# Kernel optimization log

Hardware: AMD Instinct MI355X
Metric: run time of the kernel (lower is better)

## Reference

```python
import jax, jax.numpy as jnp
import numpy as np
import math

B = 2; T = 512; ND = 256; NDAYS = 24; STRIDE = 4; KLEN = 14
DM = ND * KLEN          # 3584, d_model after unfolding
NLAYERS = 2; DSTATE = 16; DCONV = 4; EXPAND = 2
DI = EXPAND * DM        # 7168 d_inner
DTR = math.ceil(DM / 16)  # 224 dt_rank
NCLS = 41
LOUT = (T - KLEN) // STRIDE + 1  # 125


def setup_inputs():
    key = jax.random.key(0)
    ks = jax.random.split(key, 12)
    f32 = jnp.float32
    neuralInput = jax.random.normal(ks[0], (B, T, ND), f32)
    dayIdx = jax.random.randint(ks[1], (B,), 0, NDAYS)
    # day-specific linear init: identity weight, zero bias (as in BaseDecoder)
    day_w = jnp.tile(jnp.eye(ND, dtype=f32)[None], (NDAYS, 1, 1))
    day_b = jnp.zeros((NDAYS, 1, ND), f32)
    norm_w = jnp.ones((NLAYERS, DM), f32)
    norm_b = jnp.zeros((NLAYERS, DM), f32)
    in_proj_w = 0.02 * jax.random.normal(ks[2], (NLAYERS, 2 * DI, DM), f32)
    conv_w = 0.2 * jax.random.normal(ks[3], (NLAYERS, DI, DCONV), f32)  # depthwise
    conv_b = jnp.zeros((NLAYERS, DI), f32)
    x_proj_w = 0.02 * jax.random.normal(ks[4], (NLAYERS, DTR + 2 * DSTATE, DI), f32)
    s = DTR ** -0.5
    dt_proj_w = jax.random.uniform(ks[5], (NLAYERS, DI, DTR), f32, -s, s)
    # dt bias init: inverse-softplus of dt ~ LogUniform[1e-3, 1e-1]
    dt = jnp.exp(jax.random.uniform(ks[6], (NLAYERS, DI), f32) * (math.log(0.1) - math.log(0.001)) + math.log(0.001))
    dt = jnp.clip(dt, 1e-4, None)
    dt_proj_b = dt + jnp.log(-jnp.expm1(-dt))
    A_log = jnp.broadcast_to(jnp.log(jnp.arange(1, DSTATE + 1, dtype=f32)), (NLAYERS, DI, DSTATE)).copy()
    D_param = jnp.ones((NLAYERS, DI), f32)
    out_proj_w = 0.02 * jax.random.normal(ks[7], (NLAYERS, DM, DI), f32)
    normf_w = jnp.ones((DM,), f32)
    normf_b = jnp.zeros((DM,), f32)
    fc_w = 0.02 * jax.random.normal(ks[8], (NCLS, DM), f32)
    fc_b = jnp.zeros((NCLS,), f32)
    return dict(neuralInput=neuralInput, day_w=day_w, day_b=day_b, norm_w=norm_w, norm_b=norm_b,
                in_proj_w=in_proj_w, conv_w=conv_w, conv_b=conv_b, x_proj_w=x_proj_w,
                dt_proj_w=dt_proj_w, dt_proj_b=dt_proj_b, A_log=A_log, D_param=D_param,
                out_proj_w=out_proj_w, normf_w=normf_w, normf_b=normf_b, fc_w=fc_w, fc_b=fc_b,
                dayIdx=dayIdx)


def _layernorm(x, w, b):
    mu = x.mean(-1, keepdims=True)
    v = jnp.var(x, -1, keepdims=True)
    return (x - mu) * jax.lax.rsqrt(v + 1e-5) * w + b


def _mamba(h, ipw, cw, cb, xpw, dtw, dtb, Alog, Dp, opw):
    # h: (B, L, DM) -> (B, L, DM); unidirectional Mamba, use_fast_path=False math
    Bb, L, _ = h.shape
    xz = h @ ipw.T                              # (B, L, 2*DI)
    x, z = xz[..., :DI], xz[..., DI:]
    # depthwise causal conv1d, kernel DCONV, left pad DCONV-1, truncated to L
    xp = jnp.pad(x, ((0, 0), (DCONV - 1, 0), (0, 0)))
    xc = cb + sum(xp[:, j:j + L, :] * cw[:, j] for j in range(DCONV))
    x = jax.nn.silu(xc)
    x_dbl = x @ xpw.T                           # (B, L, DTR + 2*N)
    dt = x_dbl[..., :DTR]
    Bc = x_dbl[..., DTR:DTR + DSTATE]
    Cc = x_dbl[..., DTR + DSTATE:]
    delta = jax.nn.softplus(dt @ dtw.T + dtb)   # (B, L, DI), delta_softplus=True
    A = -jnp.exp(Alog)                          # (DI, N)
    dA = jnp.exp(delta[..., None] * A)          # (B, L, DI, N)
    dBu = (delta * x)[..., None] * Bc[:, :, None, :]  # (B, L, DI, N)

    def step(hst, inp):
        a, bu, c = inp
        hst = a * hst + bu                      # (B, DI, N)
        return hst, jnp.einsum('bdn,bn->bd', hst, c)

    h0 = jnp.zeros((Bb, DI, DSTATE), h.dtype)
    _, ys = jax.lax.scan(step, h0, (dA.transpose(1, 0, 2, 3), dBu.transpose(1, 0, 2, 3), Cc.transpose(1, 0, 2)))
    y = ys.transpose(1, 0, 2) + x * Dp          # skip term D*u
    y = y * jax.nn.silu(z)                      # gated output
    return y @ opw.T


def reference(neuralInput, day_w, day_b, norm_w, norm_b, in_proj_w, conv_w, conv_b, x_proj_w,
              dt_proj_w, dt_proj_b, A_log, D_param, out_proj_w, normf_w, normf_b, fc_w, fc_b, dayIdx):
    # --- BaseDecoder.forward_preprocessing (gaussianSmoothWidth = 0) ---
    t = jnp.einsum('btd,bdk->btk', neuralInput, day_w[dayIdx]) + day_b[dayIdx]
    t = t / (1.0 + jnp.abs(t))                  # Softsign
    idx = jnp.arange(LOUT)[:, None] * STRIDE + jnp.arange(KLEN)[None, :]
    win = t[:, idx, :]                          # (B, LOUT, KLEN, ND)
    # torch Unfold feature ordering: channel-major then kernel position -> d*KLEN + j
    h = win.transpose(0, 1, 3, 2).reshape(t.shape[0], LOUT, DM)
    # --- stacked Mamba blocks (pre-norm residual) ---
    residual = None
    for i in range(NLAYERS):
        residual = h if residual is None else h + residual
        hn = _layernorm(residual, norm_w[i], norm_b[i])
        h = _mamba(hn, in_proj_w[i], conv_w[i], conv_b[i], x_proj_w[i], dt_proj_w[i],
                   dt_proj_b[i], A_log[i], D_param[i], out_proj_w[i])
    residual = h + residual
    hn = _layernorm(residual, normf_w, normf_b)
    return hn @ fc_w.T + fc_b                   # (B, LOUT, NCLS)
```

## Files before the change

### kernel.cpp

```cpp
#include <hip/hip_runtime.h>
#include <hip/hip_bf16.h>
#include <math.h>

#define BATCH   2
#define TSEQ    512
#define NDIM    256
#define STRIDE_ 4
#define KLEN    14
#define DM      3584
#define DI      7168
#define DTR     224
#define DSTATE  16
#define NCLS    41
#define LOUT    125
#define LPAD    128
#define MROWS   256

typedef __attribute__((ext_vector_type(8))) short bf8_t;
typedef __attribute__((ext_vector_type(4))) float f4_t;

__device__ inline unsigned bfpair(float a, float b) {
    unsigned ua = __builtin_bit_cast(unsigned, a);
    unsigned ub = __builtin_bit_cast(unsigned, b);
    ua = (ua + 0x7fffu + ((ua >> 16) & 1u)) >> 16;
    ub = (ub + 0x7fffu + ((ub >> 16) & 1u)) >> 16;
    return ua | (ub << 16);
}
__device__ inline uint4 pack8(float4 a, float4 b) {
    return make_uint4(bfpair(a.x, a.y), bfpair(a.z, a.w),
                      bfpair(b.x, b.y), bfpair(b.z, b.w));
}

__global__ void day_proj(const float* __restrict__ nI, const float* __restrict__ dw,
                         const float* __restrict__ db, const int* __restrict__ dayIdx,
                         float* __restrict__ t_full) {
    int bi = blockIdx.x;
    int b = bi >> 9;
    int di = dayIdx[b];
    int tid = threadIdx.x;
    __shared__ float a_sh[256];
    a_sh[tid] = nI[(size_t)bi * 256 + tid];
    __syncthreads();
    const float* w = dw + (size_t)di * 65536;
    float acc = db[(size_t)di * 256 + tid];
    #pragma unroll 8
    for (int d = 0; d < 256; ++d) acc = fmaf(a_sh[d], w[d * 256 + tid], acc);
    t_full[(size_t)bi * 256 + tid] = acc / (1.f + fabsf(acc));
}

__global__ void window_k(const float* __restrict__ t_full, float* __restrict__ res) {
    int bl = blockIdx.x;
    int b = bl >> 7, l = bl & 127;
    size_t m = (size_t)b * LPAD + l;
    if (l >= LOUT) {
        for (int c = threadIdx.x; c < DM; c += 256) res[m * DM + c] = 0.f;
        return;
    }
    for (int c = threadIdx.x; c < DM; c += 256) {
        int d = c / KLEN, j = c - d * KLEN;
        res[m * DM + c] = t_full[((size_t)b * TSEQ + l * STRIDE_ + j) * 256 + d];
    }
}

template <bool ADD>
__global__ void ln_pack(float* __restrict__ res, const float* __restrict__ part,
                        const float* __restrict__ w, const float* __restrict__ b,
                        short* __restrict__ hnp) {
    __shared__ __align__(16) float hs[DM];
    __shared__ float sm[8];
    int m = blockIdx.x, tid = threadIdx.x;
    float* row = res + (size_t)m * DM;
    float s = 0.f, ss = 0.f;
    for (int c = tid; c < DM; c += 256) {
        float v = row[c];
        if (ADD) {
            v += part[((size_t)0 * MROWS + m) * DM + c]
               + part[((size_t)1 * MROWS + m) * DM + c]
               + part[((size_t)2 * MROWS + m) * DM + c]
               + part[((size_t)3 * MROWS + m) * DM + c];
            row[c] = v;
        }
        hs[c] = v; s += v; ss += v * v;
    }
    #pragma unroll
    for (int o = 32; o; o >>= 1) { s += __shfl_xor(s, o); ss += __shfl_xor(ss, o); }
    int wid = tid >> 6;
    if ((tid & 63) == 0) { sm[wid] = s; sm[4 + wid] = ss; }
    __syncthreads();
    s = sm[0] + sm[1] + sm[2] + sm[3];
    ss = sm[4] + sm[5] + sm[6] + sm[7];
    float mu = s * (1.f / DM);
    float var = ss * (1.f / DM) - mu * mu;
    float rs = rsqrtf(var + 1e-5f);
    for (int G = tid; G < DM / 8; G += 256) {
        float4 f0 = *(const float4*)(hs + G * 8);
        float4 f1 = *(const float4*)(hs + G * 8 + 4);
        float4 w0 = *(const float4*)(w + G * 8);
        float4 w1 = *(const float4*)(w + G * 8 + 4);
        float4 b0 = *(const float4*)(b + G * 8);
        float4 b1 = *(const float4*)(b + G * 8 + 4);
        f0.x = (f0.x - mu) * rs * w0.x + b0.x; f0.y = (f0.y - mu) * rs * w0.y + b0.y;
        f0.z = (f0.z - mu) * rs * w0.z + b0.z; f0.w = (f0.w - mu) * rs * w0.w + b0.w;
        f1.x = (f1.x - mu) * rs * w1.x + b1.x; f1.y = (f1.y - mu) * rs * w1.y + b1.y;
        f1.z = (f1.z - mu) * rs * w1.z + b1.z; f1.w = (f1.w - mu) * rs * w1.w + b1.w;
        *(uint4*)&hnp[((size_t)G * 256 + m) * 8] = pack8(f0, f1);
    }
}

template <int EPI, int NT>
__global__ __launch_bounds__(256)
void gemm_mfma(const short* __restrict__ Ap, const float* __restrict__ W, int ldw,
               float* __restrict__ C, int ldc, int kSteps, size_t cStrideZ,
               const float* __restrict__ bias) {
    constexpr int NC = NT / 16;
    __shared__ __align__(16) short a_sh[3][4][2056];
    __shared__ __align__(16) short w_sh[3][4][NT * 8 + 8];
    const int tid = threadIdx.x;
    const int wz = tid >> 6, lane = tid & 63;
    const int g = lane >> 4, i16 = lane & 15;
    const int n0 = blockIdx.x * NT;
    const int sBeg = blockIdx.z * kSteps, sEnd = sBeg + kSteps;
    const int wr = tid >> 3;
    const int wq = tid & 7;
    C += (size_t)blockIdx.z * cStrideZ;

    f4_t acc[4][NC];
    #pragma unroll
    for (int r = 0; r < 4; ++r)
        #pragma unroll
        for (int c = 0; c < NC; ++c) acc[r][c] = (f4_t){0.f, 0.f, 0.f, 0.f};

    const short* arow = Ap + (size_t)tid * 8;
    const float* wbase = W + (size_t)(n0 + wr) * ldw + wq * 4;

    auto stageA = [&](int s, int buf) {
        #pragma unroll
        for (int it = 0; it < 4; ++it)
            __builtin_amdgcn_global_load_lds(
                (const __attribute__((address_space(1))) unsigned int*)(arow + (size_t)(s * 4 + it) * 2048),
                (__attribute__((address_space(3))) unsigned int*)&a_sh[buf][it][tid * 8], 16, 0, 0);
    };

    stageA(sBeg, 0);
    float4 wv0 = *(const float4*)(wbase + (size_t)sBeg * 32);
    stageA(sBeg + 1, 1);
    float4 wv1 = *(const float4*)(wbase + (size_t)(sBeg + 1) * 32);
    {
        uint2 p0 = {bfpair(wv0.x, wv0.y), bfpair(wv0.z, wv0.w)};
        *(uint2*)&w_sh[0][wq >> 1][wr * 8 + (wq & 1) * 4] = p0;
    }
    asm volatile("s_waitcnt vmcnt(5) lgkmcnt(0)" ::: "memory");
    __builtin_amdgcn_s_barrier();

    float4 wv2;
    for (int t = sBeg; t < sEnd; ++t) {
        const int cur = (t - sBeg) % 3;
        const bool has2 = (t + 2 < sEnd);
        if (has2) {
            stageA(t + 2, (cur + 2) % 3);
            wv2 = *(const float4*)(wbase + (size_t)(t + 2) * 32);
        }
        bf8_t af[4], wf[NC];
        #pragma unroll
        for (int r = 0; r < 4; ++r)
            af[r] = *(const bf8_t*)&a_sh[cur][g][(wz * 64 + r * 16 + i16) * 8];
        #pragma unroll
        for (int c = 0; c < NC; ++c)
            wf[c] = *(const bf8_t*)&w_sh[cur][g][(c * 16 + i16) * 8];
        #pragma unroll
        for (int r = 0; r < 4; ++r)
            #pragma unroll
            for (int c = 0; c < NC; ++c)
                acc[r][c] = __builtin_amdgcn_mfma_f32_16x16x32_bf16(af[r], wf[c], acc[r][c], 0, 0, 0);
        if (t + 1 < sEnd) {
            uint2 p1 = {bfpair(wv1.x, wv1.y), bfpair(wv1.z, wv1.w)};
            *(uint2*)&w_sh[(cur + 1) % 3][wq >> 1][wr * 8 + (wq & 1) * 4] = p1;
            if (has2) {
                wv1 = wv2;
                asm volatile("s_waitcnt vmcnt(5) lgkmcnt(0)" ::: "memory");
            } else {
                asm volatile("s_waitcnt vmcnt(0) lgkmcnt(0)" ::: "memory");
            }
            __builtin_amdgcn_s_barrier();
        }
    }

    float bv[NC];
    if (EPI == 1) {
        #pragma unroll
        for (int c = 0; c < NC; ++c) bv[c] = bias[n0 + c * 16 + i16];
    }
    #pragma unroll
    for (int r = 0; r < 4; ++r) {
        #pragma unroll
        for (int c = 0; c < NC; ++c) {
            int n = n0 + c * 16 + i16;
            #pragma unroll
            for (int v = 0; v < 4; ++v) {
                int m = wz * 64 + r * 16 + g * 4 + v;
                float val = acc[r][c][v];
                if (EPI == 0) {
                    C[(size_t)m * ldc + n] = val;
                } else {
                    val += bv[c];
                    C[(size_t)m * ldc + n] = (val > 20.f) ? val : log1pf(expf(val));
                }
            }
        }
    }
}

__global__ void reduce_pack_bc(const float* __restrict__ part, float* __restrict__ xdbl,
                               short* __restrict__ xdblp) {
    int m = blockIdx.x, tid = threadIdx.x;
    float v = 0.f;
    #pragma unroll 4
    for (int z = 0; z < 28; ++z) v += part[((size_t)z * MROWS + m) * 256 + tid];
    xdbl[(size_t)m * 256 + tid] = v;
    __shared__ float buf[256];
    buf[tid] = v;
    __syncthreads();
    if (tid < DTR / 8) {
        float4 f0 = *(const float4*)&buf[tid * 8];
        float4 f1 = *(const float4*)&buf[tid * 8 + 4];
        *(uint4*)&xdblp[((size_t)tid * 256 + m) * 8] = pack8(f0, f1);
    }
}

__global__ void conv_silu_pack(const float* __restrict__ xz, const float* __restrict__ cw,
                               const float* __restrict__ cb, float* __restrict__ xq,
                               short* __restrict__ xqp) {
    int bl = blockIdx.x;
    int b = bl / 125, l = bl % 125;
    size_t m = (size_t)b * LPAD + l;
    for (int c0 = threadIdx.x * 8; c0 < DI; c0 += 2048) {
        float v[8];
        float4 cb0 = *(const float4*)(cb + c0);
        float4 cb1 = *(const float4*)(cb + c0 + 4);
        v[0] = cb0.x; v[1] = cb0.y; v[2] = cb0.z; v[3] = cb0.w;
        v[4] = cb1.x; v[5] = cb1.y; v[6] = cb1.z; v[7] = cb1.w;
        #pragma unroll
        for (int j = 0; j < 4; ++j) {
            int lj = l - 3 + j;
            if (lj < 0) continue;
            const float* xr = xz + ((size_t)b * LPAD + lj) * (2 * DI) + c0;
            float4 x0 = *(const float4*)xr;
            float4 x1 = *(const float4*)(xr + 4);
            float xa[8] = {x0.x, x0.y, x0.z, x0.w, x1.x, x1.y, x1.z, x1.w};
            #pragma unroll
            for (int k = 0; k < 8; ++k)
                v[k] = fmaf(xa[k], cw[(c0 + k) * 4 + j], v[k]);
        }
        float4 o0, o1;
        #pragma unroll
        for (int k = 0; k < 8; ++k) {
            float sv = v[k] / (1.f + expf(-v[k]));
            if (k < 4) (&o0.x)[k] = sv; else (&o1.x)[k - 4] = sv;
        }
        *(float4*)(xq + m * DI + c0) = o0;
        *(float4*)(xq + m * DI + c0 + 4) = o1;
        *(uint4*)&xqp[(((size_t)c0 / 8) * 256 + m) * 8] = pack8(o0, o1);
    }
}

__global__ void scan_kernel(const float* __restrict__ delta, const float* __restrict__ xq,
                            const float* __restrict__ xdbl, const float* __restrict__ xz,
                            const float* __restrict__ Alog, const float* __restrict__ Dp,
                            float* __restrict__ y, short* __restrict__ ybp) {
    int tid = threadIdx.x;
    int sg = tid & 3;
    int c = blockIdx.x * 64 + (tid >> 2);
    int b = blockIdx.y;
    float As[4], st[4];
    #pragma unroll
    for (int k = 0; k < 4; ++k) {
        As[k] = -expf(Alog[(size_t)c * DSTATE + sg * 4 + k]);
        st[k] = 0.f;
    }
    float dp = Dp[c];
    size_t mb = (size_t)b * LPAD;
    float d_c = delta[mb * DI + c];
    float x_c = xq[mb * DI + c];
    float z_c = xz[mb * (2 * DI) + DI + c];
    float4 B_c = *(const float4*)(xdbl + mb * 256 + DTR + sg * 4);
    float4 C_c = *(const float4*)(xdbl + mb * 256 + DTR + DSTATE + sg * 4);
    for (int l = 0; l < LOUT; ++l) {
        float d_n = d_c, x_n = x_c, z_n = z_c;
        float4 B_n = B_c, C_n = C_c;
        if (l + 1 < LOUT) {
            size_t m = mb + l + 1;
            d_n = delta[m * DI + c];
            x_n = xq[m * DI + c];
            z_n = xz[m * (2 * DI) + DI + c];
            B_n = *(const float4*)(xdbl + m * 256 + DTR + sg * 4);
            C_n = *(const float4*)(xdbl + m * 256 + DTR + DSTATE + sg * 4);
        }
        float du = d_c * x_c;
        float yv = 0.f;
        #pragma unroll
        for (int k = 0; k < 4; ++k) {
            st[k] = fmaf(expf(d_c * As[k]), st[k], du * (&B_c.x)[k]);
            yv = fmaf(st[k], (&C_c.x)[k], yv);
        }
        yv += __shfl_xor(yv, 1);
        yv += __shfl_xor(yv, 2);
        if (sg == 0) {
            float yout = (yv + x_c * dp) * (z_c / (1.f + expf(-z_c)));
            size_t m = mb + l;
            y[m * DI + c] = yout;
            ybp[((size_t)(c >> 3) * 256 + m) * 8 + (c & 7)] =
                (short)(bfpair(yout, 0.f) & 0xffffu);
        }
        d_c = d_n; x_c = x_n; z_c = z_n; B_c = B_n; C_c = C_n;
    }
}

__global__ void ln_fc(const float* __restrict__ res, const float* __restrict__ part,
                      const float* __restrict__ wf, const float* __restrict__ bf,
                      const float* __restrict__ fcw, const float* __restrict__ fcb,
                      float* __restrict__ out) {
    __shared__ __align__(16) float hs[DM];
    __shared__ float sm[8];
    int bl = blockIdx.x;
    int b = bl / 125, l = bl % 125;
    size_t m = (size_t)b * LPAD + l;
    int tid = threadIdx.x;
    const float* row = res + m * DM;
    float s = 0.f, ss = 0.f;
    for (int c = tid; c < DM; c += 256) {
        float v = row[c]
                + part[((size_t)0 * MROWS + m) * DM + c]
                + part[((size_t)1 * MROWS + m) * DM + c]
                + part[((size_t)2 * MROWS + m) * DM + c]
                + part[((size_t)3 * MROWS + m) * DM + c];
        hs[c] = v; s += v; ss += v * v;
    }
    #pragma unroll
    for (int o = 32; o; o >>= 1) { s += __shfl_xor(s, o); ss += __shfl_xor(ss, o); }
    int wid = tid >> 6;
    if ((tid & 63) == 0) { sm[wid] = s; sm[4 + wid] = ss; }
    __syncthreads();
    s = sm[0] + sm[1] + sm[2] + sm[3];
    ss = sm[4] + sm[5] + sm[6] + sm[7];
    float mu = s * (1.f / DM);
    float var = ss * (1.f / DM) - mu * mu;
    float rs = rsqrtf(var + 1e-5f);
    for (int c = tid; c < DM; c += 256) hs[c] = (hs[c] - mu) * rs * wf[c] + bf[c];
    __syncthreads();
    int lane = tid & 63;
    for (int n = wid; n < NCLS; n += 4) {
        const float* wrow = fcw + (size_t)n * DM;
        float a0 = 0.f, a1 = 0.f, a2 = 0.f, a3 = 0.f;
        for (int k = lane; k < DM; k += 256) {
            a0 = fmaf(hs[k],       wrow[k],       a0);
            a1 = fmaf(hs[k + 64],  wrow[k + 64],  a1);
            a2 = fmaf(hs[k + 128], wrow[k + 128], a2);
            a3 = fmaf(hs[k + 192], wrow[k + 192], a3);
        }
        float acc = (a0 + a1) + (a2 + a3);
        #pragma unroll
        for (int o = 32; o; o >>= 1) acc += __shfl_xor(acc, o);
        if (lane == 0) out[((size_t)b * LOUT + l) * NCLS + n] = acc + fcb[n];
    }
}

extern "C" void kernel_launch(void* const* d_in, const int* in_sizes, int n_in,
                              void* d_out, int out_size, void* d_ws, size_t ws_size,
                              hipStream_t stream) {
    (void)in_sizes; (void)n_in; (void)out_size; (void)ws_size;
    const float* nI   = (const float*)d_in[0];
    const float* dw   = (const float*)d_in[1];
    const float* db   = (const float*)d_in[2];
    const float* nw   = (const float*)d_in[3];
    const float* nb   = (const float*)d_in[4];
    const float* ipw  = (const float*)d_in[5];
    const float* cw   = (const float*)d_in[6];
    const float* cb   = (const float*)d_in[7];
    const float* xpw  = (const float*)d_in[8];
    const float* dtw  = (const float*)d_in[9];
    const float* dtb  = (const float*)d_in[10];
    const float* Alog = (const float*)d_in[11];
    const float* Dp   = (const float*)d_in[12];
    const float* opw  = (const float*)d_in[13];
    const float* nfw  = (const float*)d_in[14];
    const float* nfb  = (const float*)d_in[15];
    const float* fcw  = (const float*)d_in[16];
    const float* fcb  = (const float*)d_in[17];
    const int*   dayI = (const int*)d_in[18];
    float* out = (float*)d_out;

    float* wsf = (float*)d_ws;
    float* t_full   = wsf; wsf += 262144;
    float* res      = wsf; wsf += (size_t)MROWS * DM;
    float* xz       = wsf; wsf += (size_t)MROWS * 2 * DI;
    float* xq       = wsf; wsf += (size_t)MROWS * DI;
    float* xdbl     = wsf; wsf += (size_t)MROWS * 256;
    float* delta    = wsf; wsf += (size_t)MROWS * DI;
    float* yb       = wsf; wsf += (size_t)MROWS * DI;
    float* xdbl_prt = wsf; wsf += (size_t)28 * MROWS * 256;
    float* res_prt  = wsf; wsf += (size_t)4 * MROWS * DM;
    short* wss = (short*)wsf;
    short* hnp   = wss; wss += (size_t)MROWS * DM;
    short* xqp   = wss; wss += (size_t)MROWS * DI;
    short* xdblp = wss; wss += (size_t)MROWS * DTR;
    short* ybp   = wss; wss += (size_t)MROWS * DI;

    day_proj<<<dim3(BATCH * TSEQ), 256, 0, stream>>>(nI, dw, db, dayI, t_full);
    window_k<<<dim3(MROWS), 256, 0, stream>>>(t_full, res);

    for (int i = 0; i < 2; ++i) {
        if (i == 0)
            ln_pack<false><<<dim3(MROWS), 256, 0, stream>>>(
                res, nullptr, nw, nb, hnp);
        else
            ln_pack<true><<<dim3(MROWS), 256, 0, stream>>>(
                res, res_prt, nw + (size_t)DM, nb + (size_t)DM, hnp);
        gemm_mfma<0, 32><<<dim3(448, 1, 1), 256, 0, stream>>>(
            hnp, ipw + (size_t)i * 2 * DI * DM, DM, xz, 2 * DI, 112, 0, nullptr);
        conv_silu_pack<<<dim3(BATCH * LOUT), 256, 0, stream>>>(
            xz, cw + (size_t)i * DI * 4, cb + (size_t)i * DI, xq, xqp);
        gemm_mfma<0, 32><<<dim3(8, 1, 28), 256, 0, stream>>>(
            xqp, xpw + (size_t)i * 256 * DI, DI, xdbl_prt, 256, 8,
            (size_t)MROWS * 256, nullptr);
        reduce_pack_bc<<<dim3(MROWS), 256, 0, stream>>>(xdbl_prt, xdbl, xdblp);
        gemm_mfma<1, 32><<<dim3(224, 1, 1), 256, 0, stream>>>(
            xdblp, dtw + (size_t)i * DI * DTR, DTR, delta, DI, 7, 0, dtb + (size_t)i * DI);
        scan_kernel<<<dim3(DI / 64, BATCH), 256, 0, stream>>>(
            delta, xq, xdbl, xz, Alog + (size_t)i * DI * DSTATE, Dp + (size_t)i * DI, yb, ybp);
        gemm_mfma<0, 32><<<dim3(112, 1, 4), 256, 0, stream>>>(
            ybp, opw + (size_t)i * DM * DI, DI, res_prt, DM, 56,
            (size_t)MROWS * DM, nullptr);
    }

    ln_fc<<<dim3(BATCH * LOUT), 256, 0, stream>>>(res, res_prt, nfw, nfb, fcw, fcb, out);
}
```

Measured before the change: 1.287 ms.

## Widen GEMM N-tile to 64, fuse windowing into layernorm, drop unused scan output

The MFMA GEMM template now handles NT=64 by loading and packing two weight row groups per stage. Every GEMM launch switches to 64-wide tiles with half the blocks, which halves the re-reads of the bf16 A operand per output column. The separate window kernel is removed: ln_pack gathers the unfolded input straight from t_full, and in the second layer recomputes it before adding the partial sums. The scan no longer writes an unused fp32 y buffer. The trade-off is fewer blocks than CUs on several GEMMs, plus more registers and loads in flight per thread.

```diff
diff --git a/kernel.cpp b/kernel.cpp
--- a/kernel.cpp
+++ b/kernel.cpp
@@ -48,37 +48,28 @@
     t_full[(size_t)bi * 256 + tid] = acc / (1.f + fabsf(acc));
 }
 
-__global__ void window_k(const float* __restrict__ t_full, float* __restrict__ res) {
-    int bl = blockIdx.x;
-    int b = bl >> 7, l = bl & 127;
-    size_t m = (size_t)b * LPAD + l;
-    if (l >= LOUT) {
-        for (int c = threadIdx.x; c < DM; c += 256) res[m * DM + c] = 0.f;
-        return;
-    }
-    for (int c = threadIdx.x; c < DM; c += 256) {
-        int d = c / KLEN, j = c - d * KLEN;
-        res[m * DM + c] = t_full[((size_t)b * TSEQ + l * STRIDE_ + j) * 256 + d];
-    }
-}
-
-template <bool ADD>
-__global__ void ln_pack(float* __restrict__ res, const float* __restrict__ part,
-                        const float* __restrict__ w, const float* __restrict__ b,
-                        short* __restrict__ hnp) {
+template <int MODE>
+__global__ void ln_pack(const float* __restrict__ t_full, float* __restrict__ res,
+                        const float* __restrict__ part, const float* __restrict__ w,
+                        const float* __restrict__ b, short* __restrict__ hnp) {
     __shared__ __align__(16) float hs[DM];
     __shared__ float sm[8];
     int m = blockIdx.x, tid = threadIdx.x;
-    float* row = res + (size_t)m * DM;
+    int bb = m >> 7, l = m & 127;
+    const float* tb = t_full + ((size_t)bb * TSEQ + (size_t)l * STRIDE_) * 256;
     float s = 0.f, ss = 0.f;
     for (int c = tid; c < DM; c += 256) {
-        float v = row[c];
-        if (ADD) {
+        float v = 0.f;
+        if (l < LOUT) {
+            int d = c / KLEN, j = c - d * KLEN;
+            v = tb[(size_t)j * 256 + d];
+        }
+        if (MODE == 1) {
             v += part[((size_t)0 * MROWS + m) * DM + c]
                + part[((size_t)1 * MROWS + m) * DM + c]
                + part[((size_t)2 * MROWS + m) * DM + c]
                + part[((size_t)3 * MROWS + m) * DM + c];
-            row[c] = v;
+            res[(size_t)m * DM + c] = v;
         }
         hs[c] = v; s += v; ss += v * v;
     }
@@ -131,7 +122,8 @@
         for (int c = 0; c < NC; ++c) acc[r][c] = (f4_t){0.f, 0.f, 0.f, 0.f};
 
     const short* arow = Ap + (size_t)tid * 8;
-    const float* wbase = W + (size_t)(n0 + wr) * ldw + wq * 4;
+    const float* wbase  = W + (size_t)(n0 + wr) * ldw + wq * 4;
+    const float* wbase2 = wbase + (size_t)32 * ldw;
 
     auto stageA = [&](int s, int buf) {
         #pragma unroll
@@ -140,25 +132,41 @@
                 (const __attribute__((address_space(1))) unsigned int*)(arow + (size_t)(s * 4 + it) * 2048),
                 (__attribute__((address_space(3))) unsigned int*)&a_sh[buf][it][tid * 8], 16, 0, 0);
     };
+    auto packW = [&](int buf, float4 wa, float4 wb) {
+        uint2 p0 = {bfpair(wa.x, wa.y), bfpair(wa.z, wa.w)};
+        *(uint2*)&w_sh[buf][wq >> 1][wr * 8 + (wq & 1) * 4] = p0;
+        if constexpr (NT == 64) {
+            uint2 p1 = {bfpair(wb.x, wb.y), bfpair(wb.z, wb.w)};
+            *(uint2*)&w_sh[buf][wq >> 1][(wr + 32) * 8 + (wq & 1) * 4] = p1;
+        }
+    };
+
+    float4 wa0, wa1, wa2;
+    float4 wb0 = make_float4(0.f, 0.f, 0.f, 0.f);
+    float4 wb1 = wb0, wb2 = wb0;
 
     stageA(sBeg, 0);
-    float4 wv0 = *(const float4*)(wbase + (size_t)sBeg * 32);
+    wa0 = *(const float4*)(wbase + (size_t)sBeg * 32);
+    if constexpr (NT == 64) wb0 = *(const float4*)(wbase2 + (size_t)sBeg * 32);
     stageA(sBeg + 1, 1);
-    float4 wv1 = *(const float4*)(wbase + (size_t)(sBeg + 1) * 32);
-    {
-        uint2 p0 = {bfpair(wv0.x, wv0.y), bfpair(wv0.z, wv0.w)};
-        *(uint2*)&w_sh[0][wq >> 1][wr * 8 + (wq & 1) * 4] = p0;
-    }
-    asm volatile("s_waitcnt vmcnt(5) lgkmcnt(0)" ::: "memory");
+    wa1 = *(const float4*)(wbase + (size_t)(sBeg + 1) * 32);
+    if constexpr (NT == 64) wb1 = *(const float4*)(wbase2 + (size_t)(sBeg + 1) * 32);
+    packW(0, wa0, wb0);
+    if constexpr (NT == 64)
+        asm volatile("s_waitcnt vmcnt(6) lgkmcnt(0)" ::: "memory");
+    else
+        asm volatile("s_waitcnt vmcnt(5) lgkmcnt(0)" ::: "memory");
     __builtin_amdgcn_s_barrier();
 
-    float4 wv2;
+    int cur = 0;
     for (int t = sBeg; t < sEnd; ++t) {
-        const int cur = (t - sBeg) % 3;
+        const int nb = (cur == 2) ? 0 : cur + 1;
+        const int pb = (nb == 2) ? 0 : nb + 1;
         const bool has2 = (t + 2 < sEnd);
         if (has2) {
-            stageA(t + 2, (cur + 2) % 3);
-            wv2 = *(const float4*)(wbase + (size_t)(t + 2) * 32);
+            stageA(t + 2, pb);
+            wa2 = *(const float4*)(wbase + (size_t)(t + 2) * 32);
+            if constexpr (NT == 64) wb2 = *(const float4*)(wbase2 + (size_t)(t + 2) * 32);
         }
         bf8_t af[4], wf[NC];
         #pragma unroll
@@ -173,16 +181,19 @@
             for (int c = 0; c < NC; ++c)
                 acc[r][c] = __builtin_amdgcn_mfma_f32_16x16x32_bf16(af[r], wf[c], acc[r][c], 0, 0, 0);
         if (t + 1 < sEnd) {
-            uint2 p1 = {bfpair(wv1.x, wv1.y), bfpair(wv1.z, wv1.w)};
-            *(uint2*)&w_sh[(cur + 1) % 3][wq >> 1][wr * 8 + (wq & 1) * 4] = p1;
+            packW(nb, wa1, wb1);
+            wa1 = wa2; wb1 = wb2;
             if (has2) {
-                wv1 = wv2;
-                asm volatile("s_waitcnt vmcnt(5) lgkmcnt(0)" ::: "memory");
+                if constexpr (NT == 64)
+                    asm volatile("s_waitcnt vmcnt(6) lgkmcnt(0)" ::: "memory");
+                else
+                    asm volatile("s_waitcnt vmcnt(5) lgkmcnt(0)" ::: "memory");
             } else {
                 asm volatile("s_waitcnt vmcnt(0) lgkmcnt(0)" ::: "memory");
             }
             __builtin_amdgcn_s_barrier();
         }
+        cur = nb;
     }
 
     float bv[NC];
@@ -266,7 +277,7 @@
 __global__ void scan_kernel(const float* __restrict__ delta, const float* __restrict__ xq,
                             const float* __restrict__ xdbl, const float* __restrict__ xz,
                             const float* __restrict__ Alog, const float* __restrict__ Dp,
-                            float* __restrict__ y, short* __restrict__ ybp) {
+                            short* __restrict__ ybp) {
     int tid = threadIdx.x;
     int sg = tid & 3;
     int c = blockIdx.x * 64 + (tid >> 2);
@@ -307,7 +318,6 @@
         if (sg == 0) {
             float yout = (yv + x_c * dp) * (z_c / (1.f + expf(-z_c)));
             size_t m = mb + l;
-            y[m * DI + c] = yout;
             ybp[((size_t)(c >> 3) * 256 + m) * 8 + (c & 7)] =
                 (short)(bfpair(yout, 0.f) & 0xffffu);
         }
@@ -396,7 +406,6 @@
     float* xq       = wsf; wsf += (size_t)MROWS * DI;
     float* xdbl     = wsf; wsf += (size_t)MROWS * 256;
     float* delta    = wsf; wsf += (size_t)MROWS * DI;
-    float* yb       = wsf; wsf += (size_t)MROWS * DI;
     float* xdbl_prt = wsf; wsf += (size_t)28 * MROWS * 256;
     float* res_prt  = wsf; wsf += (size_t)4 * MROWS * DM;
     short* wss = (short*)wsf;
@@ -406,28 +415,27 @@
     short* ybp   = wss; wss += (size_t)MROWS * DI;
 
     day_proj<<<dim3(BATCH * TSEQ), 256, 0, stream>>>(nI, dw, db, dayI, t_full);
-    window_k<<<dim3(MROWS), 256, 0, stream>>>(t_full, res);
 
     for (int i = 0; i < 2; ++i) {
         if (i == 0)
-            ln_pack<false><<<dim3(MROWS), 256, 0, stream>>>(
-                res, nullptr, nw, nb, hnp);
+            ln_pack<0><<<dim3(MROWS), 256, 0, stream>>>(
+                t_full, res, nullptr, nw, nb, hnp);
         else
-            ln_pack<true><<<dim3(MROWS), 256, 0, stream>>>(
-                res, res_prt, nw + (size_t)DM, nb + (size_t)DM, hnp);
-        gemm_mfma<0, 32><<<dim3(448, 1, 1), 256, 0, stream>>>(
+            ln_pack<1><<<dim3(MROWS), 256, 0, stream>>>(
+                t_full, res, res_prt, nw + (size_t)DM, nb + (size_t)DM, hnp);
+        gemm_mfma<0, 64><<<dim3(224, 1, 1), 256, 0, stream>>>(
             hnp, ipw + (size_t)i * 2 * DI * DM, DM, xz, 2 * DI, 112, 0, nullptr);
         conv_silu_pack<<<dim3(BATCH * LOUT), 256, 0, stream>>>(
             xz, cw + (size_t)i * DI * 4, cb + (size_t)i * DI, xq, xqp);
-        gemm_mfma<0, 32><<<dim3(8, 1, 28), 256, 0, stream>>>(
+        gemm_mfma<0, 64><<<dim3(4, 1, 28), 256, 0, stream>>>(
             xqp, xpw + (size_t)i * 256 * DI, DI, xdbl_prt, 256, 8,
             (size_t)MROWS * 256, nullptr);
         reduce_pack_bc<<<dim3(MROWS), 256, 0, stream>>>(xdbl_prt, xdbl, xdblp);
-        gemm_mfma<1, 32><<<dim3(224, 1, 1), 256, 0, stream>>>(
+        gemm_mfma<1, 64><<<dim3(112, 1, 1), 256, 0, stream>>>(
             xdblp, dtw + (size_t)i * DI * DTR, DTR, delta, DI, 7, 0, dtb + (size_t)i * DI);
         scan_kernel<<<dim3(DI / 64, BATCH), 256, 0, stream>>>(
-            delta, xq, xdbl, xz, Alog + (size_t)i * DI * DSTATE, Dp + (size_t)i * DI, yb, ybp);
-        gemm_mfma<0, 32><<<dim3(112, 1, 4), 256, 0, stream>>>(
+            delta, xq, xdbl, xz, Alog + (size_t)i * DI * DSTATE, Dp + (size_t)i * DI, ybp);
+        gemm_mfma<0, 64><<<dim3(56, 1, 4), 256, 0, stream>>>(
             ybp, opw + (size_t)i * DM * DI, DI, res_prt, DM, 56,
             (size_t)MROWS * DM, nullptr);
     }
```

Result: slower. 1.368 ms (+6.2%).
